# Optimization experiments

Measured on AMD Instinct MI355X. Metric: run time of the kernel, lower is better.

## Reference

```python
import jax, jax.numpy as jnp
import numpy as np

ALPHA = 0.2  # LeakyReLU negative slope


def setup_inputs() -> dict:
    key = jax.random.key(0)
    k1, k2, k3, k4 = jax.random.split(key, 4)
    B, Cin, Cout, N, T, Kt = 8, 64, 64, 2048, 13, 3
    L = T - Kt + 1  # 11, must equal `length`
    x = jax.random.normal(k1, (B, Cin, N, T), dtype=jnp.float32)
    w0 = jax.random.normal(k2, (Cout, Cin, 1, Kt), dtype=jnp.float32) * 0.05
    b0 = jax.random.normal(k3, (Cout,), dtype=jnp.float32) * 0.05
    w1 = jax.random.normal(k4, (Cout * L,), dtype=jnp.float32) * 0.05
    return {"x": x, "w0": w0, "b0": b0, "w1": w1}


def reference(x, w0, b0, w1):
    # conv0: Conv2d(in,out,(1,Kt)), VALID padding -> [B, Cout, N, L]
    h = jax.lax.conv_general_dilated(
        x, w0, window_strides=(1, 1), padding='VALID',
        dimension_numbers=('NCHW', 'OIHW', 'NCHW')) + b0[None, :, None, None]
    B, C, N, L = h.shape
    # permute(0,1,3,2).view(B, C*L, N) then 1x1 Conv1d (no bias) == contraction over (c,l)
    # NOTE: original module uses conv1 for BOTH f_1 and f_2 (conv2 unused), so f_1 == f_2.
    f = jnp.einsum('bcnl,cl->bn', h, w1.reshape(C, L))  # [B, N]
    logits = f[:, :, None] + f[:, None, :]              # [B, N, N]
    lrelu = jnp.where(logits >= 0, logits, ALPHA * logits)
    attention = jax.nn.softmax(lrelu, axis=-1)          # softmax over last (column) dim
    attention = jnp.swapaxes(attention, -1, -2)         # [B, N, N] transposed
    # h_prime[b,c,q,l] = sum_n h[b,c,n,l] * attention[b,n,q]
    h_prime = jnp.einsum('bcnl,bnq->bcql', h, attention)
    return h_prime, attention
```

## Files before the change

### kernel.cpp

```cpp
#include <hip/hip_runtime.h>

#define BB 8
#define CIN 64
#define COUT 64
#define NN 2048
#define TT 13
#define KTT 3
#define LL 11
#define CL 704
#define HP_SIZE 11534336LL

#define WS_TAB_OFF 65568ULL
#define WS_W0PK_OFF 327712ULL
#define WS_APAN_OFF 352288ULL

typedef _Float16 f16;
typedef __attribute__((ext_vector_type(8))) _Float16 f16x8;
typedef __attribute__((ext_vector_type(2))) _Float16 f16x2;
typedef __attribute__((ext_vector_type(4))) float f32x4;

__device__ __forceinline__ unsigned int pk16(float a, float b) {
  f16 ha = (f16)a, hb = (f16)b;
  unsigned short ua = __builtin_bit_cast(unsigned short, ha);
  unsigned short ub = __builtin_bit_cast(unsigned short, hb);
  return (unsigned int)ua | ((unsigned int)ub << 16);
}
__device__ __forceinline__ f16x2 as_h2(unsigned int u) {
  return __builtin_bit_cast(f16x2, u);
}

__global__ __launch_bounds__(256) void k_pack(const float* __restrict__ w0,
                                              unsigned int* __restrict__ w0pk_g) {
  int tid = blockIdx.x * 256 + threadIdx.x;
  int c = tid & 63, r = tid >> 6;
  int kt = r % 3, cip = r / 3;
  float ev = w0[c * 192 + cip * 6 + kt];
  float od = w0[c * 192 + cip * 6 + 3 + kt];
  w0pk_g[r * 64 + c] = pk16(ev, od);
}

__global__ __launch_bounds__(512, 6) void k_conv(
    const float* __restrict__ x, const unsigned int* __restrict__ w0pk_g,
    const float* __restrict__ b0, const float* __restrict__ w1,
    f16* __restrict__ Apan, float* __restrict__ f) {
  __shared__ unsigned int w0pk[96 * 64];
  __shared__ unsigned int xspk[32 * 8 * 16];
  __shared__ f16 As[704 * 8];
  const int tid = threadIdx.x;
  const int b = blockIdx.x >> 8;
  const int n0 = (blockIdx.x & 255) << 3;

#pragma unroll
  for (int i = 0; i < 12; ++i) w0pk[i * 512 + tid] = w0pk_g[i * 512 + tid];

#pragma unroll
  for (int i = 0; i < 7; ++i) {
    int task = i * 512 + tid;
    if (task < 3328) {
      int cip = task / 104, rem = task - cip * 104;
      long long base = (long long)(b * 64 + 2 * cip) * 26624 + n0 * 13 + rem;
      float ev = x[base];
      float od = x[base + 26624];
      int n = rem / 13, t = rem - n * 13;
      xspk[(cip * 8 + n) * 16 + t] = pk16(ev, od);
    }
  }
  __syncthreads();

  const int c = tid & 63, w = tid >> 6;
  float acc[11];
  const float bias = b0[c];
#pragma unroll
  for (int l = 0; l < 11; ++l) acc[l] = bias;

  for (int cip = 0; cip < 32; ++cip) {
    const unsigned int* xr = &xspk[(cip * 8 + w) * 16];
    uint4 xa = *(const uint4*)xr;
    uint4 xb = *(const uint4*)(xr + 4);
    uint4 xc = *(const uint4*)(xr + 8);
    unsigned int x13[13] = {xa.x, xa.y, xa.z, xa.w, xb.x, xb.y, xb.z, xb.w,
                            xc.x, xc.y, xc.z, xc.w, xr[12]};
    f16x2 wk0 = as_h2(w0pk[(cip * 3 + 0) * 64 + c]);
    f16x2 wk1 = as_h2(w0pk[(cip * 3 + 1) * 64 + c]);
    f16x2 wk2 = as_h2(w0pk[(cip * 3 + 2) * 64 + c]);
#pragma unroll
    for (int l = 0; l < 11; ++l) {
      acc[l] = __builtin_amdgcn_fdot2(as_h2(x13[l]), wk0, acc[l], false);
      acc[l] = __builtin_amdgcn_fdot2(as_h2(x13[l + 1]), wk1, acc[l], false);
      acc[l] = __builtin_amdgcn_fdot2(as_h2(x13[l + 2]), wk2, acc[l], false);
    }
  }

  float p = 0.f;
#pragma unroll
  for (int l = 0; l < 11; ++l) p = fmaf(acc[l], w1[c * 11 + l], p);
#pragma unroll
  for (int off = 32; off; off >>= 1) p += __shfl_xor(p, off, 64);
  if (c == 0) f[b * 2048 + n0 + w] = p;

#pragma unroll
  for (int l = 0; l < 11; ++l) As[(c * 11 + l) * 8 + w] = (f16)acc[l];
  __syncthreads();

  const int ks = n0 >> 5, kgrp = (n0 >> 3) & 3;
#pragma unroll
  for (int i = 0; i < 2; ++i) {
    int m = i * 512 + tid;
    if (m < 704) {
      uint4 v = *(const uint4*)&As[m * 8];
      int mt = m >> 6, fr = (m >> 4) & 3, r16 = m & 15;
      long long base = ((long long)(b * 11 + mt) * 64 + ks) * 2048 +
                       fr * 512 + (kgrp * 16 + r16) * 8;
      *(uint4*)&Apan[base] = v;
    }
  }
}

__global__ __launch_bounds__(256) void k_maxf(const float* __restrict__ f,
                                              float* __restrict__ maxf) {
  const int b = blockIdx.x, tid = threadIdx.x;
  float m = -1e30f;
  for (int i = tid; i < 2048; i += 256) m = fmaxf(m, f[b * 2048 + i]);
#pragma unroll
  for (int off = 32; off; off >>= 1) m = fmaxf(m, __shfl_xor(m, off, 64));
  __shared__ float red[4];
  if ((tid & 63) == 0) red[tid >> 6] = m;
  __syncthreads();
  if (tid == 0) maxf[b] = fmaxf(fmaxf(red[0], red[1]), fmaxf(red[2], red[3]));
}

__global__ __launch_bounds__(256) void k_rowsum(const float* __restrict__ f,
                                                const float* __restrict__ maxf,
                                                float4* __restrict__ tab4) {
  __shared__ float fs[2048];
  const int b = blockIdx.x >> 9;
  const int q0 = (blockIdx.x & 511) << 2;
  const int tid = threadIdx.x;
#pragma unroll
  for (int i = 0; i < 8; ++i) fs[i * 256 + tid] = f[b * 2048 + i * 256 + tid];
  __syncthreads();
  const int lane = tid & 63, wid = tid >> 6;
  const int q = q0 + wid;
  const float fq = fs[q];
  const float mb = maxf[b];
  float t = fq + mb;
  const float m = t >= 0.f ? t : 0.2f * t;
  float sum = 0.f;
  for (int j = lane; j < 2048; j += 64) {
    float v = fq + fs[j];
    v = v >= 0.f ? v : 0.2f * v;
    sum += __expf(v - m);
  }
#pragma unroll
  for (int off = 32; off; off >>= 1) sum += __shfl_xor(sum, off, 64);
  if (lane == 0) {
    float rq = 1.0f / sum;
    float En = __expf(fq - mb);
    float E2 = __expf(0.2f * fq);
    float Rq = t >= 0.f ? rq : rq * __expf(0.8f * t);
    float Sq = rq * __expf(0.2f * fq - m);
    tab4[b * 2048 + q] = make_float4(En, E2, Rq, Sq);
  }
}

__global__ __launch_bounds__(256, 3) void k_gemm(const f16* __restrict__ Apan,
                                                 const float4* __restrict__ tab4,
                                                 float* __restrict__ att,
                                                 float* __restrict__ out) {
  __shared__ __align__(16) float2 Etab[2048];

  const int p = blockIdx.x;
  const int g = p % 88, qt = p / 88;
  const int b = g / 11, mt = g % 11;

  const int tid = threadIdx.x;
  const int qw = tid >> 6, lane = tid & 63;
  const int l15 = lane & 15, l4 = lane >> 4;

  const f16* Ab = Apan + ((long long)(b * 11 + mt) * 64) * 2048 + lane * 8;
  const float4* tb = tab4 + (long long)b * NN;

#pragma unroll
  for (int i = 0; i < 8; ++i) {
    int idx = i * 256 + tid;
    float4 v = tb[idx];
    Etab[idx] = make_float2(v.x, v.y);
  }
  const int q0 = qt * 256 + qw * 64 + l15;
  float Rq0, Sq0, Rq1, Sq1, Rq2, Sq2, Rq3, Sq3;
  { float4 t4 = tb[q0];      Rq0 = t4.z; Sq0 = t4.w; }
  { float4 t4 = tb[q0 + 16]; Rq1 = t4.z; Sq1 = t4.w; }
  { float4 t4 = tb[q0 + 32]; Rq2 = t4.z; Sq2 = t4.w; }
  { float4 t4 = tb[q0 + 48]; Rq3 = t4.z; Sq3 = t4.w; }
  __syncthreads();

  f32x4 acc[4][4];
#pragma unroll
  for (int fr = 0; fr < 4; ++fr)
#pragma unroll
    for (int nf = 0; nf < 4; ++nf) acc[fr][nf] = (f32x4){0.f, 0.f, 0.f, 0.f};

  f16x8 c0 = *(const f16x8*)(Ab);
  f16x8 c1 = *(const f16x8*)(Ab + 512);
  f16x8 c2 = *(const f16x8*)(Ab + 1024);
  f16x8 c3 = *(const f16x8*)(Ab + 1536);

  for (int ks = 0; ks < 64; ++ks) {
    f16x8 n0 = c0, n1 = c1, n2 = c2, n3 = c3;
    if (ks < 63) {
      const f16* at = Ab + (ks + 1) * 2048;
      n0 = *(const f16x8*)(at);
      n1 = *(const f16x8*)(at + 512);
      n2 = *(const f16x8*)(at + 1024);
      n3 = *(const f16x8*)(at + 1536);
    }
    const int nb = ks * 32 + l4 * 8;
    const float4* ep = (const float4*)&Etab[nb];
    float4 e0 = ep[0], e1 = ep[1], e2 = ep[2], e3 = ep[3];
    float En[8] = {e0.x, e0.z, e1.x, e1.z, e2.x, e2.z, e3.x, e3.z};
    float E2[8] = {e0.y, e0.w, e1.y, e1.w, e2.y, e2.w, e3.y, e3.w};
    const bool owned = ((ks * 11) >> 6) == mt;
    const long long abase = ((long long)(b * 2048 + nb)) * 2048 + q0;

    f16x8 bv0, bv1, bv2, bv3;
    float vf[4][8];
#pragma unroll
    for (int u = 0; u < 8; ++u) {
      float v0 = fmaxf(En[u] * Rq0, E2[u] * Sq0);
      float v1 = fmaxf(En[u] * Rq1, E2[u] * Sq1);
      float v2 = fmaxf(En[u] * Rq2, E2[u] * Sq2);
      float v3 = fmaxf(En[u] * Rq3, E2[u] * Sq3);
      vf[0][u] = v0; vf[1][u] = v1; vf[2][u] = v2; vf[3][u] = v3;
      bv0[u] = (f16)v0; bv1[u] = (f16)v1; bv2[u] = (f16)v2; bv3[u] = (f16)v3;
    }
    if (owned) {
#pragma unroll
      for (int nf = 0; nf < 4; ++nf) {
        float* ap = att + abase + nf * 16;
#pragma unroll
        for (int u = 0; u < 8; ++u) ap[(long long)u * 2048] = vf[nf][u];
      }
    }
    __builtin_amdgcn_s_setprio(1);
    acc[0][0] = __builtin_amdgcn_mfma_f32_16x16x32_f16(c0, bv0, acc[0][0], 0, 0, 0);
    acc[1][0] = __builtin_amdgcn_mfma_f32_16x16x32_f16(c1, bv0, acc[1][0], 0, 0, 0);
    acc[2][0] = __builtin_amdgcn_mfma_f32_16x16x32_f16(c2, bv0, acc[2][0], 0, 0, 0);
    acc[3][0] = __builtin_amdgcn_mfma_f32_16x16x32_f16(c3, bv0, acc[3][0], 0, 0, 0);
    acc[0][1] = __builtin_amdgcn_mfma_f32_16x16x32_f16(c0, bv1, acc[0][1], 0, 0, 0);
    acc[1][1] = __builtin_amdgcn_mfma_f32_16x16x32_f16(c1, bv1, acc[1][1], 0, 0, 0);
    acc[2][1] = __builtin_amdgcn_mfma_f32_16x16x32_f16(c2, bv1, acc[2][1], 0, 0, 0);
    acc[3][1] = __builtin_amdgcn_mfma_f32_16x16x32_f16(c3, bv1, acc[3][1], 0, 0, 0);
    acc[0][2] = __builtin_amdgcn_mfma_f32_16x16x32_f16(c0, bv2, acc[0][2], 0, 0, 0);
    acc[1][2] = __builtin_amdgcn_mfma_f32_16x16x32_f16(c1, bv2, acc[1][2], 0, 0, 0);
    acc[2][2] = __builtin_amdgcn_mfma_f32_16x16x32_f16(c2, bv2, acc[2][2], 0, 0, 0);
    acc[3][2] = __builtin_amdgcn_mfma_f32_16x16x32_f16(c3, bv2, acc[3][2], 0, 0, 0);
    acc[0][3] = __builtin_amdgcn_mfma_f32_16x16x32_f16(c0, bv3, acc[0][3], 0, 0, 0);
    acc[1][3] = __builtin_amdgcn_mfma_f32_16x16x32_f16(c1, bv3, acc[1][3], 0, 0, 0);
    acc[2][3] = __builtin_amdgcn_mfma_f32_16x16x32_f16(c2, bv3, acc[2][3], 0, 0, 0);
    acc[3][3] = __builtin_amdgcn_mfma_f32_16x16x32_f16(c3, bv3, acc[3][3], 0, 0, 0);
    __builtin_amdgcn_s_setprio(0);

    c0 = n0; c1 = n1; c2 = n2; c3 = n3;
  }

  float* ob = out + (long long)b * COUT * NN * LL;
#pragma unroll
  for (int fr = 0; fr < 4; ++fr) {
#pragma unroll
    for (int r = 0; r < 4; ++r) {
      int m = mt * 64 + fr * 16 + l4 * 4 + r;
      int c = m / 11, l2 = m - c * 11;
      float* orow = ob + (long long)c * NN * LL + l2;
#pragma unroll
      for (int nf = 0; nf < 4; ++nf) {
        int q = q0 + nf * 16;
        orow[(long long)q * LL] = acc[fr][nf][r];
      }
    }
  }
}

extern "C" void kernel_launch(void* const* d_in, const int* in_sizes, int n_in,
                              void* d_out, int out_size, void* d_ws, size_t ws_size,
                              hipStream_t stream) {
  const float* x  = (const float*)d_in[0];
  const float* w0 = (const float*)d_in[1];
  const float* b0 = (const float*)d_in[2];
  const float* w1 = (const float*)d_in[3];

  float* fbuf = (float*)d_ws;
  float* maxf = fbuf + BB * NN;
  float4* tab4 = (float4*)((char*)d_ws + WS_TAB_OFF);
  unsigned int* w0pk_g = (unsigned int*)((char*)d_ws + WS_W0PK_OFF);
  f16* Apan = (f16*)((char*)d_ws + WS_APAN_OFF);

  float* hp  = (float*)d_out;
  float* att = hp + HP_SIZE;

  k_pack<<<dim3(24), dim3(256), 0, stream>>>(w0, w0pk_g);
  k_conv<<<dim3(BB * 256), dim3(512), 0, stream>>>(x, w0pk_g, b0, w1, Apan, fbuf);
  k_maxf<<<dim3(BB), dim3(256), 0, stream>>>(fbuf, maxf);
  k_rowsum<<<dim3(BB * 512), dim3(256), 0, stream>>>(fbuf, maxf, tab4);
  k_gemm<<<dim3(704), dim3(256), 0, stream>>>(Apan, tab4, att, hp);
}
```

Before: 151.1 us.

## Compute conv0 with MFMA 16x16x32 f16 instead of packed fdot2

Rewrites the temporal convolution kernel to use matrix-core MFMA instructions. Weights are pre-packed into per-lane A fragments and the input is staged per node as fp16 with zero-padded time columns; each wave builds B fragments by im2col over (ci,kt) with the output time on the N dimension. This replaces the scalar dot2 loops, aiming to cut conv ALU time, at the cost of padding waste (16 columns for 11 outputs), more shared memory and lower occupancy (launch bound 4 instead of 6). Bias and w1 are now staged in shared memory for the epilogue.

```diff
diff --git a/kernel.cpp b/kernel.cpp
--- a/kernel.cpp
+++ b/kernel.cpp
@@ -11,7 +11,7 @@
 #define HP_SIZE 11534336LL
 
 #define WS_TAB_OFF 65568ULL
-#define WS_W0PK_OFF 327712ULL
+#define WS_WFRAG_OFF 327712ULL
 #define WS_APAN_OFF 352288ULL
 
 typedef _Float16 f16;
@@ -29,77 +29,97 @@
   return __builtin_bit_cast(f16x2, u);
 }
 
-__global__ __launch_bounds__(256) void k_pack(const float* __restrict__ w0,
-                                              unsigned int* __restrict__ w0pk_g) {
-  int tid = blockIdx.x * 256 + threadIdx.x;
-  int c = tid & 63, r = tid >> 6;
-  int kt = r % 3, cip = r / 3;
-  float ev = w0[c * 192 + cip * 6 + kt];
-  float od = w0[c * 192 + cip * 6 + 3 + kt];
-  w0pk_g[r * 64 + c] = pk16(ev, od);
-}
-
-__global__ __launch_bounds__(512, 6) void k_conv(
-    const float* __restrict__ x, const unsigned int* __restrict__ w0pk_g,
+__global__ __launch_bounds__(256) void k_pack2(const float* __restrict__ w0,
+                                               f16* __restrict__ w0frag) {
+  int t = blockIdx.x * 256 + threadIdx.x;
+  int lane = t & 63, sc = t >> 6;
+  int s = sc >> 2, cf = sc & 3;
+  int l4 = lane >> 4, l15 = lane & 15;
+  int c = cf * 16 + l15;
+  const float* src = w0 + c * 192 + s * 32 + l4 * 8;
+  f16x8 v;
+#pragma unroll
+  for (int u = 0; u < 8; ++u) v[u] = (f16)src[u];
+  *(f16x8*)&w0frag[(long long)t * 8] = v;
+}
+
+__global__ __launch_bounds__(512, 4) void k_conv(
+    const float* __restrict__ x, const f16* __restrict__ w0frag_g,
     const float* __restrict__ b0, const float* __restrict__ w1,
     f16* __restrict__ Apan, float* __restrict__ f) {
-  __shared__ unsigned int w0pk[96 * 64];
-  __shared__ unsigned int xspk[32 * 8 * 16];
-  __shared__ f16 As[704 * 8];
+  __shared__ __align__(16) f16 wfr[24 * 64 * 8];
+  __shared__ f16 xs16[8 * 64 * 18];
+  __shared__ __align__(16) f16 As[704 * 8];
+  __shared__ float w1s[704];
+  __shared__ float b0s[64];
   const int tid = threadIdx.x;
   const int b = blockIdx.x >> 8;
   const int n0 = (blockIdx.x & 255) << 3;
 
-#pragma unroll
-  for (int i = 0; i < 12; ++i) w0pk[i * 512 + tid] = w0pk_g[i * 512 + tid];
-
-#pragma unroll
-  for (int i = 0; i < 7; ++i) {
+  {
+    const uint4* src = (const uint4*)w0frag_g;
+    uint4* dst = (uint4*)wfr;
+#pragma unroll
+    for (int i = 0; i < 3; ++i) dst[i * 512 + tid] = src[i * 512 + tid];
+  }
+  for (int i = tid; i < 704; i += 512) w1s[i] = w1[i];
+  if (tid < 64) b0s[tid] = b0[tid];
+#pragma unroll
+  for (int i = 0; i < 13; ++i) {
     int task = i * 512 + tid;
-    if (task < 3328) {
-      int cip = task / 104, rem = task - cip * 104;
-      long long base = (long long)(b * 64 + 2 * cip) * 26624 + n0 * 13 + rem;
-      float ev = x[base];
-      float od = x[base + 26624];
-      int n = rem / 13, t = rem - n * 13;
-      xspk[(cip * 8 + n) * 16 + t] = pk16(ev, od);
-    }
-  }
-  __syncthreads();
-
-  const int c = tid & 63, w = tid >> 6;
-  float acc[11];
-  const float bias = b0[c];
-#pragma unroll
-  for (int l = 0; l < 11; ++l) acc[l] = bias;
-
-  for (int cip = 0; cip < 32; ++cip) {
-    const unsigned int* xr = &xspk[(cip * 8 + w) * 16];
-    uint4 xa = *(const uint4*)xr;
-    uint4 xb = *(const uint4*)(xr + 4);
-    uint4 xc = *(const uint4*)(xr + 8);
-    unsigned int x13[13] = {xa.x, xa.y, xa.z, xa.w, xb.x, xb.y, xb.z, xb.w,
-                            xc.x, xc.y, xc.z, xc.w, xr[12]};
-    f16x2 wk0 = as_h2(w0pk[(cip * 3 + 0) * 64 + c]);
-    f16x2 wk1 = as_h2(w0pk[(cip * 3 + 1) * 64 + c]);
-    f16x2 wk2 = as_h2(w0pk[(cip * 3 + 2) * 64 + c]);
-#pragma unroll
-    for (int l = 0; l < 11; ++l) {
-      acc[l] = __builtin_amdgcn_fdot2(as_h2(x13[l]), wk0, acc[l], false);
-      acc[l] = __builtin_amdgcn_fdot2(as_h2(x13[l + 1]), wk1, acc[l], false);
-      acc[l] = __builtin_amdgcn_fdot2(as_h2(x13[l + 2]), wk2, acc[l], false);
+    int ci = task / 104, rem = task - ci * 104;
+    int n = rem / 13, t2 = rem - n * 13;
+    float v = x[(long long)(b * 64 + ci) * 26624 + n0 * 13 + rem];
+    xs16[(n * 64 + ci) * 18 + t2] = (f16)v;
+  }
+  for (int task = tid; task < 2560; task += 512) {
+    int p5 = task % 5, rest = task / 5;
+    xs16[rest * 18 + 13 + p5] = (f16)0.f;
+  }
+  __syncthreads();
+
+  const int lane = tid & 63, w = tid >> 6;
+  const int l4 = lane >> 4, l15 = lane & 15;
+  const f16* xn = &xs16[w * 1152];
+
+  f32x4 acc[4];
+#pragma unroll
+  for (int cf = 0; cf < 4; ++cf) acc[cf] = (f32x4){0.f, 0.f, 0.f, 0.f};
+
+#pragma unroll
+  for (int s = 0; s < 6; ++s) {
+    int k0 = s * 32 + l4 * 8;
+    int ci = k0 / 3, kt = k0 - ci * 3;
+    f16x8 bf;
+#pragma unroll
+    for (int u = 0; u < 8; ++u) {
+      bf[u] = xn[ci * 18 + kt + l15];
+      ++kt;
+      if (kt == 3) { kt = 0; ++ci; }
+    }
+#pragma unroll
+    for (int cf = 0; cf < 4; ++cf) {
+      f16x8 af = *(const f16x8*)&wfr[((s * 4 + cf) * 64 + lane) * 8];
+      acc[cf] = __builtin_amdgcn_mfma_f32_16x16x32_f16(af, bf, acc[cf], 0, 0, 0);
     }
   }
 
   float p = 0.f;
 #pragma unroll
-  for (int l = 0; l < 11; ++l) p = fmaf(acc[l], w1[c * 11 + l], p);
+  for (int cf = 0; cf < 4; ++cf) {
+#pragma unroll
+    for (int r = 0; r < 4; ++r) {
+      int c = cf * 16 + l4 * 4 + r;
+      float hv = acc[cf][r] + b0s[c];
+      if (l15 < 11) {
+        p = fmaf(hv, w1s[c * 11 + l15], p);
+        As[(c * 11 + l15) * 8 + w] = (f16)hv;
+      }
+    }
+  }
 #pragma unroll
   for (int off = 32; off; off >>= 1) p += __shfl_xor(p, off, 64);
-  if (c == 0) f[b * 2048 + n0 + w] = p;
-
-#pragma unroll
-  for (int l = 0; l < 11; ++l) As[(c * 11 + l) * 8 + w] = (f16)acc[l];
+  if (lane == 0) f[b * 2048 + n0 + w] = p;
   __syncthreads();
 
   const int ks = n0 >> 5, kgrp = (n0 >> 3) & 3;
@@ -291,14 +311,14 @@
   float* fbuf = (float*)d_ws;
   float* maxf = fbuf + BB * NN;
   float4* tab4 = (float4*)((char*)d_ws + WS_TAB_OFF);
-  unsigned int* w0pk_g = (unsigned int*)((char*)d_ws + WS_W0PK_OFF);
+  f16* w0frag = (f16*)((char*)d_ws + WS_WFRAG_OFF);
   f16* Apan = (f16*)((char*)d_ws + WS_APAN_OFF);
 
   float* hp  = (float*)d_out;
   float* att = hp + HP_SIZE;
 
-  k_pack<<<dim3(24), dim3(256), 0, stream>>>(w0, w0pk_g);
-  k_conv<<<dim3(BB * 256), dim3(512), 0, stream>>>(x, w0pk_g, b0, w1, Apan, fbuf);
+  k_pack2<<<dim3(6), dim3(256), 0, stream>>>(w0, w0frag);
+  k_conv<<<dim3(BB * 256), dim3(512), 0, stream>>>(x, w0frag, b0, w1, Apan, fbuf);
   k_maxf<<<dim3(BB), dim3(256), 0, stream>>>(fbuf, maxf);
   k_rowsum<<<dim3(BB * 512), dim3(256), 0, stream>>>(fbuf, maxf, tab4);
   k_gemm<<<dim3(704), dim3(256), 0, stream>>>(Apan, tab4, att, hp);
```

Measured after the change: 138.5 us. 8.3% less time.
